# Performance work log

Hardware: AMD Instinct MI355X
Metric: run time of the kernel (lower is better)

## Reference

```python
import jax, jax.numpy as jnp
import numpy as np

B, L, D = 4, 4096, 1024
H = 16
BS = 64                      # block_size
HD = D // H                  # head_dim = 64
NB = L // BS                 # num_blocks = 64 (L multiple of BS -> no padding)
SCALE = HD ** -0.5
TEMP = 0.7
N_SINK_ITERS = 7


def setup_inputs() -> dict:
    key = jax.random.key(0)
    ks = jax.random.split(key, 7)
    x = jax.random.normal(ks[0], (B, L, D), dtype=jnp.float32)
    # gumbel noise matching torch.rand_like(log_alpha) -> -log(-log(u+eps)+eps)
    u = jax.random.uniform(ks[1], (B, H, NB, NB), dtype=jnp.float32)
    gumbel = -jnp.log(-jnp.log(u + 1e-20) + 1e-20)
    s_in = 1.0 / np.sqrt(D)
    W_qkv = jax.random.normal(ks[2], (D, 3 * D), dtype=jnp.float32) * s_in
    b_qkv = jnp.zeros((3 * D,), dtype=jnp.float32)
    W_out = jax.random.normal(ks[3], (D, D), dtype=jnp.float32) * s_in
    b_out = jnp.zeros((D,), dtype=jnp.float32)
    return {"x": x, "gumbel": gumbel, "W_qkv": W_qkv, "b_qkv": b_qkv,
            "W_out": W_out, "b_out": b_out}


def _sinkhorn(log_alpha):
    # Gumbel noise already added by caller; iterate row/col log-normalization.
    for _ in range(N_SINK_ITERS):
        log_alpha = log_alpha - jax.nn.logsumexp(log_alpha, axis=-1, keepdims=True)
        log_alpha = log_alpha - jax.nn.logsumexp(log_alpha, axis=-2, keepdims=True)
    return jnp.exp(log_alpha)


def reference(x, gumbel, W_qkv, b_qkv, W_out, b_out):
    qkv = x @ W_qkv + b_qkv                              # [B,L,3D]
    q, k, v = jnp.split(qkv, 3, axis=-1)

    def to_blocks(t):  # [B,L,D] -> [B,H,NB,BS,HD]
        return t.reshape(B, L, H, HD).transpose(0, 2, 1, 3).reshape(B, H, NB, BS, HD)

    q_b, k_b, v_b = to_blocks(q), to_blocks(k), to_blocks(v)

    # block summaries and Gumbel-Sinkhorn permutation over blocks
    q_repr = q_b.mean(axis=3)                            # [B,H,NB,HD]
    k_repr = k_b.mean(axis=3)
    sim = jnp.einsum('bhnd,bhmd->bhnm', q_repr, k_repr) * SCALE
    P = _sinkhorn((sim + gumbel) / TEMP)                 # [B,H,NB,NB]

    # sort K/V blocks via soft permutation
    k_flat = k_b.reshape(B, H, NB, BS * HD)
    v_flat = v_b.reshape(B, H, NB, BS * HD)
    k_sorted = jnp.einsum('bhnm,bhmf->bhnf', P, k_flat).reshape(B, H, NB, BS, HD)
    v_sorted = jnp.einsum('bhnm,bhmf->bhnf', P, v_flat).reshape(B, H, NB, BS, HD)

    # block i attends to [own block, sorted block i+1]; last block only to itself
    k_next = jnp.roll(k_sorted, -1, axis=2)
    v_next = jnp.roll(v_sorted, -1, axis=2)
    k_local = jnp.concatenate([k_b, k_next], axis=3)     # [B,H,NB,2BS,HD]
    v_local = jnp.concatenate([v_b, v_next], axis=3)

    scores = jnp.einsum('bhnqd,bhnkd->bhnqk', q_b, k_local) * SCALE
    # mask second half of keys for last block (it only attends to itself)
    scores = scores.at[:, :, -1, :, BS:].set(-1e9)
    attn = jax.nn.softmax(scores, axis=-1)               # dropout: eval -> identity
    out = jnp.einsum('bhnqk,bhnkd->bhnqd', attn, v_local)

    out = out.reshape(B, H, L, HD).transpose(0, 2, 1, 3).reshape(B, L, D)
    return out @ W_out + b_out
```

## Files before the change

### kernel.cpp

```cpp
#include <hip/hip_runtime.h>
#include <cstdint>
#include <cstddef>
#include <cstdio>

#define B_   4
#define L_   4096
#define D_   1024
#define H_   16
#define BS_  64
#define HD_  64
#define NB_  64
#define SCALE_   0.125f
#define INV_TEMP (1.0f/0.7f)

typedef unsigned short bf16_t;

#ifndef __has_builtin
#define __has_builtin(x) 0
#endif
#if __has_builtin(__builtin_amdgcn_global_load_lds)
#define HAS_GLD 1
#else
#define HAS_GLD 0
#endif

#if HAS_GLD
#define GLD16(gp, lp) __builtin_amdgcn_global_load_lds(                        \
    (__attribute__((address_space(1))) void*)(uintptr_t)(gp),                  \
    (__attribute__((address_space(3))) void*)(unsigned int)(uintptr_t)(lp),    \
    16, 0, 0)
#endif

__device__ __forceinline__ float b2f(bf16_t u) {
    union { unsigned int i; float f; } c; c.i = ((unsigned int)u) << 16; return c.f;
}
__device__ __forceinline__ bf16_t f2b(float f) {
    union { float f; unsigned int i; } c; c.f = f;
    unsigned int r = c.i + 0x7FFFu + ((c.i >> 16) & 1u);
    return (bf16_t)(r >> 16);
}

__device__ __forceinline__ void storeC(float* p, float v)  { *p = v; }
__device__ __forceinline__ void storeC(bf16_t* p, float v) { *p = f2b(v); }

using bf16x8 = __attribute__((ext_vector_type(8))) short;
using f32x4  = __attribute__((ext_vector_type(4))) float;

__global__ __launch_bounds__(256) void f32_to_bf16_kernel(
    const float* __restrict__ src, bf16_t* __restrict__ dst, int n4)
{
    const int i = blockIdx.x * 256 + threadIdx.x;
    if (i < n4) {
        float4 v = *(const float4*)(src + (size_t)i * 4);
        ushort4 o = {f2b(v.x), f2b(v.y), f2b(v.z), f2b(v.w)};
        *(ushort4*)(dst + (size_t)i * 4) = o;
    }
}

__global__ __launch_bounds__(256) void transpose_f32_bf16_kernel(
    const float* __restrict__ src, bf16_t* __restrict__ dst, int R, int C)
{
    __shared__ float t[32][33];
    const int c0 = blockIdx.x * 32, r0 = blockIdx.y * 32;
    for (int i = threadIdx.y; i < 32; i += 8)
        t[i][threadIdx.x] = src[(size_t)(r0 + i) * C + c0 + threadIdx.x];
    __syncthreads();
    for (int i = threadIdx.y; i < 32; i += 8)
        dst[(size_t)(c0 + i) * R + r0 + threadIdx.x] = f2b(t[threadIdx.x][i]);
}

#if HAS_GLD
#define SGA(tt, hb, dst)                                                       \
    GLD16(gAb + (size_t)((hb) * 128) * K + (size_t)(tt) * 64,                  \
          (dst) + (((hb) * 128 + w * 16) * 64));                               \
    GLD16(gAb + (size_t)((hb) * 128 + 8) * K + (size_t)(tt) * 64,              \
          (dst) + (((hb) * 128 + w * 16 + 8) * 64))
#define SGB(tt, hb, dst)                                                       \
    GLD16(gBb + (size_t)((hb) * 128) * K + (size_t)(tt) * 64,                  \
          (dst) + (((hb) * 128 + w * 16) * 64));                               \
    GLD16(gBb + (size_t)((hb) * 128 + 8) * K + (size_t)(tt) * 64,              \
          (dst) + (((hb) * 128 + w * 16 + 8) * 64))
#else
#define SGA(tt, hb, dst)                                                       \
    *(bf16x8*)((dst) + (((hb) * 128 + w * 16) * 64) + lane * 8) =              \
        *(const bf16x8*)(gAb + (size_t)((hb) * 128) * K + (size_t)(tt) * 64);  \
    *(bf16x8*)((dst) + (((hb) * 128 + w * 16 + 8) * 64) + lane * 8) =          \
        *(const bf16x8*)(gAb + (size_t)((hb) * 128 + 8) * K + (size_t)(tt) * 64)
#define SGB(tt, hb, dst)                                                       \
    *(bf16x8*)((dst) + (((hb) * 128 + w * 16) * 64) + lane * 8) =              \
        *(const bf16x8*)(gBb + (size_t)((hb) * 128) * K + (size_t)(tt) * 64);  \
    *(bf16x8*)((dst) + (((hb) * 128 + w * 16 + 8) * 64) + lane * 8) =          \
        *(const bf16x8*)(gBb + (size_t)((hb) * 128 + 8) * K + (size_t)(tt) * 64)
#endif

#define PHASE(ABUF, p, STAGE, ENDWAIT)                                         \
  {                                                                            \
    bf16x8 a0k0 = *(const bf16x8*)&(ABUF)[aRow0 + (2*(p))   * 1024 + csw[0]];  \
    bf16x8 a0k1 = *(const bf16x8*)&(ABUF)[aRow0 + (2*(p))   * 1024 + csw[1]];  \
    bf16x8 a1k0 = *(const bf16x8*)&(ABUF)[aRow0 + (2*(p)+1) * 1024 + csw[0]];  \
    bf16x8 a1k1 = *(const bf16x8*)&(ABUF)[aRow0 + (2*(p)+1) * 1024 + csw[1]];  \
    STAGE;                                                                     \
    __builtin_amdgcn_s_barrier();                                              \
    asm volatile("s_waitcnt lgkmcnt(0)" ::: "memory");                         \
    __builtin_amdgcn_s_setprio(1);                                             \
    _Pragma("unroll")                                                          \
    for (int fn = 0; fn < 4; ++fn) {                                           \
      acc[2*(p)][fn]   = __builtin_amdgcn_mfma_f32_16x16x32_bf16(              \
          a0k0, bq[fn][0], acc[2*(p)][fn], 0, 0, 0);                           \
      acc[2*(p)][fn]   = __builtin_amdgcn_mfma_f32_16x16x32_bf16(              \
          a0k1, bq[fn][1], acc[2*(p)][fn], 0, 0, 0);                           \
      acc[2*(p)+1][fn] = __builtin_amdgcn_mfma_f32_16x16x32_bf16(              \
          a1k0, bq[fn][0], acc[2*(p)+1][fn], 0, 0, 0);                         \
      acc[2*(p)+1][fn] = __builtin_amdgcn_mfma_f32_16x16x32_bf16(              \
          a1k1, bq[fn][1], acc[2*(p)+1][fn], 0, 0, 0);                         \
    }                                                                          \
    __builtin_amdgcn_s_setprio(0);                                             \
    ENDWAIT;                                                                   \
    __builtin_amdgcn_s_barrier();                                              \
    asm volatile("" ::: "memory");                                             \
  }

#define KTILE(ABUF, BBUF, NABUF, t)                                            \
  {                                                                            \
    bf16x8 bq[4][2];                                                           \
    _Pragma("unroll")                                                          \
    for (int fn = 0; fn < 4; ++fn) {                                           \
      bq[fn][0] = *(const bf16x8*)&(BBUF)[bRow0 + fn * 1024 + csw[0]];         \
      bq[fn][1] = *(const bf16x8*)&(BBUF)[bRow0 + fn * 1024 + csw[1]];         \
    }                                                                          \
    const bool stA = ((t) + 1 < KT), stB = ((t) + 2 < KT);                     \
    PHASE(ABUF, 0, if (stA) { SGA((t) + 1, 0, NABUF); }, )                     \
    PHASE(ABUF, 1, if (stA) { SGA((t) + 1, 1, NABUF); }, )                     \
    PHASE(ABUF, 2, if (stB) { SGB((t) + 2, 0, BBUF); }, )                      \
    PHASE(ABUF, 3, if (stB) { SGB((t) + 2, 1, BBUF); },                        \
          if ((t) + 1 < KT) {                                                  \
            if (stB) { asm volatile("s_waitcnt vmcnt(4)" ::: "memory"); }      \
            else     { asm volatile("s_waitcnt vmcnt(0)" ::: "memory"); }      \
          })                                                                   \
  }

template<typename TC>
__global__ __launch_bounds__(512, 2) void gemm256_8phase_kernel(
    const bf16_t* __restrict__ A, const bf16_t* __restrict__ Bt,
    const float* __restrict__ bias, TC* __restrict__ C,
    int M, int N, int K)
{
    __shared__ __align__(16) short sm[65536];
    short* const smA0 = sm;
    short* const smB0 = sm + 16384;
    short* const smA1 = sm + 32768;
    short* const smB1 = sm + 49152;

    const int tid  = threadIdx.x;
    const int lane = tid & 63;
    const int w    = tid >> 6;
    const int wr   = w >> 2, wc = w & 3;
    const int ml   = lane & 15, q2 = lane >> 4;

    const int gx  = gridDim.x;
    const int nwg = gx * gridDim.y;
    const int bid = blockIdx.y * gx + blockIdx.x;
    int swz = bid;
    if ((nwg & 7) == 0) swz = (bid & 7) * (nwg >> 3) + (bid >> 3);
    const int m0 = (swz / gx) * 256, n0 = (swz % gx) * 256;

    const int KT   = K >> 6;

    int csw[2];
    csw[0] = ((q2)     ^ (ml & 7)) * 8;
    csw[1] = ((4 + q2) ^ (ml & 7)) * 8;
    const int aRow0 = (wr * 128 + ml) * 64;
    const int bRow0 = (wc * 64  + ml) * 64;

    const int rl   = lane >> 3;
    const int scol = ((lane & 7) ^ rl) * 8;
    const bf16_t* gAb = A  + (size_t)(m0 + w * 16 + rl) * K + scol;
    const bf16_t* gBb = Bt + (size_t)(n0 + w * 16 + rl) * K + scol;

    f32x4 acc[8][4];
    #pragma unroll
    for (int i = 0; i < 8; ++i)
        #pragma unroll
        for (int j = 0; j < 4; ++j)
            acc[i][j] = {0.f, 0.f, 0.f, 0.f};

    SGA(0, 0, smA0); SGA(0, 1, smA0);
    SGB(0, 0, smB0); SGB(0, 1, smB0);
    SGB(1, 0, smB1); SGB(1, 1, smB1);
    asm volatile("s_waitcnt vmcnt(4)" ::: "memory");
    __builtin_amdgcn_s_barrier();
    asm volatile("" ::: "memory");

    for (int t = 0; t < KT; t += 2) {
        KTILE(smA0, smB0, smA1, t);
        KTILE(smA1, smB1, smA0, t + 1);
    }

    float bv[4];
    #pragma unroll
    for (int fn = 0; fn < 4; ++fn)
        bv[fn] = bias[n0 + wc * 64 + fn * 16 + ml];
    #pragma unroll
    for (int fm = 0; fm < 8; ++fm)
        #pragma unroll
        for (int fn = 0; fn < 4; ++fn)
            #pragma unroll
            for (int r = 0; r < 4; ++r) {
                const int row = m0 + wr * 128 + fm * 16 + q2 * 4 + r;
                const int col = n0 + wc * 64  + fn * 16 + ml;
                storeC(&C[(size_t)row * N + col], acc[fm][fn][r] + bv[fn]);
            }
}

#undef KTILE
#undef PHASE
#undef SGA
#undef SGB

__global__ __launch_bounds__(256) void block_repr_kernel(
    const bf16_t* __restrict__ qkv,
    float* __restrict__ q_repr, float* __restrict__ k_repr)
{
    __shared__ float red[2][4][64];
    const int blk = blockIdx.x;
    const int n  = blk & 63;
    const int bh = blk >> 6;
    const int h  = bh & 15, b = bh >> 4;
    const int d  = threadIdx.x & 63;
    const int ss = threadIdx.x >> 6;
    const bf16_t* base = qkv + (size_t)(b * L_ + n * BS_) * (3 * D_) + h * HD_ + d;
    float sq = 0.f, sk = 0.f;
    for (int s = ss; s < BS_; s += 4) {
        sq += b2f(base[(size_t)s * (3 * D_)]);
        sk += b2f(base[(size_t)s * (3 * D_) + D_]);
    }
    red[0][ss][d] = sq;
    red[1][ss][d] = sk;
    __syncthreads();
    if (threadIdx.x < 64) {
        const int dd = threadIdx.x;
        q_repr[(size_t)blk * HD_ + dd] =
            (red[0][0][dd] + red[0][1][dd] + red[0][2][dd] + red[0][3][dd])
            * (1.0f / BS_);
    } else if (threadIdx.x < 128) {
        const int dd = threadIdx.x - 64;
        k_repr[(size_t)blk * HD_ + dd] =
            (red[1][0][dd] + red[1][1][dd] + red[1][2][dd] + red[1][3][dd])
            * (1.0f / BS_);
    }
}

__global__ __launch_bounds__(256) void sinkhorn_kernel(
    const float* __restrict__ q_repr, const float* __restrict__ k_repr,
    const float* __restrict__ gumbel, bf16_t* __restrict__ P_bf)
{
    __shared__ __align__(16) float qr[64 * 68];
    __shared__ __align__(16) float kr[64 * 68];
    __shared__ float la[64 * 65];
    const int bh  = blockIdx.x;
    const int tid = threadIdx.x;
    const int r   = tid >> 2;
    const int sub = tid & 3;

    for (int idx = tid; idx < 4096; idx += 256) {
        const int rr = idx >> 6, cc = idx & 63;
        qr[rr * 68 + cc] = q_repr[(size_t)bh * 4096 + idx];
        kr[rr * 68 + cc] = k_repr[(size_t)bh * 4096 + idx];
    }
    __syncthreads();

    {
        float acc[16];
        #pragma unroll
        for (int mi = 0; mi < 16; ++mi) acc[mi] = 0.f;
        for (int d4 = 0; d4 < 16; ++d4) {
            const float4 q = *(const float4*)&qr[r * 68 + d4 * 4];
            #pragma unroll
            for (int mi = 0; mi < 16; ++mi) {
                const float4 kv = *(const float4*)&kr[(4 * mi + sub) * 68 + d4 * 4];
                acc[mi] += q.x * kv.x + q.y * kv.y + q.z * kv.z + q.w * kv.w;
            }
        }
        #pragma unroll
        for (int mi = 0; mi < 16; ++mi) {
            const int m = 4 * mi + sub;
            la[r * 65 + m] = (acc[mi] * SCALE_
                + gumbel[(size_t)bh * 4096 + r * 64 + m]) * INV_TEMP;
        }
    }
    __syncthreads();

    for (int it = 0; it < 7; ++it) {
        {
            float v[16];
            #pragma unroll
            for (int mi = 0; mi < 16; ++mi) v[mi] = la[r * 65 + 4 * mi + sub];
            float mx = v[0];
            #pragma unroll
            for (int mi = 1; mi < 16; ++mi) mx = fmaxf(mx, v[mi]);
            mx = fmaxf(mx, __shfl_xor(mx, 1, 64));
            mx = fmaxf(mx, __shfl_xor(mx, 2, 64));
            float sum = 0.f;
            #pragma unroll
            for (int mi = 0; mi < 16; ++mi) sum += expf(v[mi] - mx);
            sum += __shfl_xor(sum, 1, 64);
            sum += __shfl_xor(sum, 2, 64);
            const float lse = mx + logf(sum);
            #pragma unroll
            for (int mi = 0; mi < 16; ++mi) la[r * 65 + 4 * mi + sub] = v[mi] - lse;
        }
        __syncthreads();
        {
            float v[16];
            #pragma unroll
            for (int mi = 0; mi < 16; ++mi) v[mi] = la[(4 * mi + sub) * 65 + r];
            float mx = v[0];
            #pragma unroll
            for (int mi = 1; mi < 16; ++mi) mx = fmaxf(mx, v[mi]);
            mx = fmaxf(mx, __shfl_xor(mx, 1, 64));
            mx = fmaxf(mx, __shfl_xor(mx, 2, 64));
            float sum = 0.f;
            #pragma unroll
            for (int mi = 0; mi < 16; ++mi) sum += expf(v[mi] - mx);
            sum += __shfl_xor(sum, 1, 64);
            sum += __shfl_xor(sum, 2, 64);
            const float lse = mx + logf(sum);
            #pragma unroll
            for (int mi = 0; mi < 16; ++mi)
                la[(4 * mi + sub) * 65 + r] = v[mi] - lse;
        }
        __syncthreads();
    }

    #pragma unroll
    for (int mi = 0; mi < 16; ++mi) {
        const int m = 4 * mi + sub;
        P_bf[(size_t)bh * 4096 + r * 64 + m] = f2b(expf(la[r * 65 + m]));
    }
}

__global__ __launch_bounds__(256) void sort_kv_mfma_kernel(
    const bf16_t* __restrict__ P_bf, const bf16_t* __restrict__ qkv,
    bf16_t* __restrict__ k_sorted, bf16_t* __restrict__ v_sorted)
{
    constexpr int RS = 66;
    __shared__ __align__(16) short Kst[4 * 64 * RS];
    const int tid = threadIdx.x, lane = tid & 63, w = tid >> 6;
    const int bh = blockIdx.y;
    const int h = bh & 15, b = bh >> 4;
    const int c = blockIdx.x;
    const int ml = lane & 15, q8 = (lane >> 4) * 8;

    const bf16_t* ps = P_bf + (size_t)bh * (NB_ * NB_);

    const int s = c * 4 + w;
    const int fbase = c * 256 + w * 64;
    short* Kw = &Kst[w * 64 * RS];
    const int srow = lane >> 3;
    const int sc8  = (lane & 7) * 8;

    for (int kv = 0; kv < 2; ++kv) {
        const bf16_t* src = qkv + ((size_t)(b * L_ + s)) * (3 * D_)
                          + (kv ? 2 * D_ : 1 * D_) + h * HD_;

        #pragma unroll
        for (int g = 0; g < 8; ++g) {
            const int m = g * 8 + srow;
            *(bf16x8*)&Kw[m * RS + sc8] =
                *(const bf16x8*)(src + (size_t)m * (BS_ * 3 * D_) + sc8);
        }

        bf16x8 bt[4][2];
        #pragma unroll
        for (int kt = 0; kt < 2; ++kt)
            #pragma unroll
            for (int j = 0; j < 8; ++j) {
                const short* rp = &Kw[(kt * 32 + q8 + j) * RS + ml];
                #pragma unroll
                for (int t = 0; t < 4; ++t)
                    bt[t][kt][j] = rp[t * 16];
            }

        f32x4 acc[4][4];
        #pragma unroll
        for (int nt = 0; nt < 4; ++nt)
            #pragma unroll
            for (int t = 0; t < 4; ++t)
                acc[nt][t] = {0.f, 0.f, 0.f, 0.f};

        #pragma unroll
        for (int nt = 0; nt < 4; ++nt) {
            bf16x8 a0 = *(const bf16x8*)&ps[(size_t)(nt * 16 + ml) * 64 + q8];
            bf16x8 a1 = *(const bf16x8*)&ps[(size_t)(nt * 16 + ml) * 64 + 32 + q8];
            #pragma unroll
            for (int t = 0; t < 4; ++t) {
                acc[nt][t] = __builtin_amdgcn_mfma_f32_16x16x32_bf16(
                    a0, bt[t][0], acc[nt][t], 0, 0, 0);
                acc[nt][t] = __builtin_amdgcn_mfma_f32_16x16x32_bf16(
                    a1, bt[t][1], acc[nt][t], 0, 0, 0);
            }
        }

        bf16_t* dst = (kv ? v_sorted : k_sorted) + (size_t)bh * (NB_ * BS_ * HD_);
        const int quad4 = (lane >> 4) * 4;
        #pragma unroll
        for (int nt = 0; nt < 4; ++nt)
            #pragma unroll
            for (int t = 0; t < 4; ++t)
                #pragma unroll
                for (int r = 0; r < 4; ++r)
                    dst[(size_t)(nt * 16 + quad4 + r) * (BS_ * HD_)
                        + fbase + t * 16 + ml] = f2b(acc[nt][t][r]);
    }
}

__global__ __launch_bounds__(256) void attn_mfma_kernel(
    const bf16_t* __restrict__ qkv, const bf16_t* __restrict__ k_sorted,
    const bf16_t* __restrict__ v_sorted, bf16_t* __restrict__ attn_out)
{
    constexpr int KS = 72, VS = 136, PS = 136;
    __shared__ short Ks[128 * KS];
    __shared__ short Vt[64 * VS];
    short* const Psh = Ks;
    const int tid = threadIdx.x, lane = tid & 63, w = tid >> 6;
    const int n  = blockIdx.x & 63;
    const int bh = blockIdx.x >> 6;
    const int h = bh & 15, b = bh >> 4;
    const bool last = (n == NB_ - 1);

    const bf16_t* qb = qkv + (size_t)(b * L_ + n * BS_) * (3 * D_) + h * HD_;
    const bf16_t* kb = qb + D_;
    const bf16_t* vb = qb + 2 * D_;
    const size_t nextoff = ((size_t)bh * NB_ + (n + 1)) * (size_t)(BS_ * HD_);
    const bf16_t* kn = k_sorted + nextoff;
    const bf16_t* vn = v_sorted + nextoff;

    {
        const int col8 = (tid & 7) * 8, r0 = tid >> 3;
        const int jjmax = last ? 2 : 4;
        for (int jj = 0; jj < jjmax; ++jj) {
            const int row = jj * 32 + r0;
            const bf16_t* src = (row < 64)
                ? kb + (size_t)row * (3 * D_) + col8
                : kn + (size_t)(row - 64) * HD_ + col8;
            *(bf16x8*)&Ks[row * KS + col8] = *(const bf16x8*)src;
        }
    }
    {
        const int halves = last ? 1 : 2;
        for (int half = 0; half < halves; ++half) {
            for (int jj = 0; jj < 4; ++jj) {
                const int d0 = jj * 16 + w * 4;
                const bf16_t* src = (half == 0)
                    ? vb + (size_t)lane * (3 * D_) + d0
                    : vn + (size_t)lane * HD_ + d0;
                ushort4 u = *(const ushort4*)src;
                const int kcol = half * 64 + lane;
                Vt[(d0 + 0) * VS + kcol] = u.x;
                Vt[(d0 + 1) * VS + kcol] = u.y;
                Vt[(d0 + 2) * VS + kcol] = u.z;
                Vt[(d0 + 3) * VS + kcol] = u.w;
            }
        }
    }

    const int ml = lane & 15, quad = lane >> 4, q8 = quad * 8;
    const int m0 = w * 16;

    bf16x8 af0 = *(const bf16x8*)(qb + (size_t)(m0 + ml) * (3 * D_) + q8);
    bf16x8 af1 = *(const bf16x8*)(qb + (size_t)(m0 + ml) * (3 * D_) + 32 + q8);

    __syncthreads();

    const int ntile = last ? 4 : 8;
    f32x4 st[8];
    #pragma unroll
    for (int t = 0; t < 8; ++t) st[t] = {0.f, 0.f, 0.f, 0.f};
    for (int t = 0; t < ntile; ++t) {
        bf16x8 b0 = *(const bf16x8*)&Ks[(t * 16 + ml) * KS + q8];
        bf16x8 b1 = *(const bf16x8*)&Ks[(t * 16 + ml) * KS + 32 + q8];
        st[t] = __builtin_amdgcn_mfma_f32_16x16x32_bf16(af0, b0, st[t], 0, 0, 0);
        st[t] = __builtin_amdgcn_mfma_f32_16x16x32_bf16(af1, b1, st[t], 0, 0, 0);
    }

    __syncthreads();

    #pragma unroll
    for (int reg = 0; reg < 4; ++reg) {
        float mx = -1e30f;
        for (int t = 0; t < ntile; ++t) mx = fmaxf(mx, st[t][reg] * SCALE_);
        #pragma unroll
        for (int xm = 1; xm <= 8; xm <<= 1)
            mx = fmaxf(mx, __shfl_xor(mx, xm, 64));
        float e[8];
        float sum = 0.f;
        for (int t = 0; t < ntile; ++t) {
            e[t] = __expf(st[t][reg] * SCALE_ - mx);
            sum += e[t];
        }
        #pragma unroll
        for (int xm = 1; xm <= 8; xm <<= 1)
            sum += __shfl_xor(sum, xm, 64);
        const float inv = 1.0f / sum;
        const int qrow = m0 + quad * 4 + reg;
        for (int t = 0; t < ntile; ++t)
            Psh[qrow * PS + t * 16 + ml] = f2b(e[t] * inv);
    }

    __syncthreads();

    const int ktv = last ? 2 : 4;
    f32x4 oacc[4];
    #pragma unroll
    for (int t = 0; t < 4; ++t) oacc[t] = {0.f, 0.f, 0.f, 0.f};
    for (int kt = 0; kt < ktv; ++kt) {
        bf16x8 pa = *(const bf16x8*)&Psh[(m0 + ml) * PS + kt * 32 + q8];
        #pragma unroll
        for (int t = 0; t < 4; ++t) {
            bf16x8 vf = *(const bf16x8*)&Vt[(t * 16 + ml) * VS + kt * 32 + q8];
            oacc[t] = __builtin_amdgcn_mfma_f32_16x16x32_bf16(pa, vf, oacc[t], 0, 0, 0);
        }
    }

    bf16_t* ob = attn_out + (size_t)(b * L_ + n * BS_) * D_ + h * HD_;
    #pragma unroll
    for (int t = 0; t < 4; ++t)
        #pragma unroll
        for (int reg = 0; reg < 4; ++reg) {
            const int qrow = m0 + quad * 4 + reg;
            ob[(size_t)qrow * D_ + t * 16 + ml] = f2b(oacc[t][reg]);
        }
}

extern "C" void kernel_launch(void* const* d_in, const int* in_sizes, int n_in,
                              void* d_out, int out_size, void* d_ws, size_t ws_size,
                              hipStream_t stream)
{
    const float* x      = (const float*)d_in[0];
    const float* gumbel = (const float*)d_in[1];
    const float* W_qkv  = (const float*)d_in[2];
    const float* b_qkv  = (const float*)d_in[3];
    const float* W_out  = (const float*)d_in[4];
    const float* b_out  = (const float*)d_in[5];
    float* out = (float*)d_out;

    const size_t need = 204472320ull;
    if (ws_size < need) {
        fprintf(stderr, "[kernel_launch] ws_size=%zu < need=%zu — aborting launch\n",
                ws_size, need);
        return;
    }

    bf16_t* qkv      = (bf16_t*)d_ws;
    bf16_t* attn_o   = qkv    + (size_t)B_ * L_ * 3 * D_;
    bf16_t* k_sorted = attn_o + (size_t)B_ * L_ * D_;
    bf16_t* v_sorted = k_sorted + (size_t)B_ * L_ * D_;
    float* q_repr    = (float*)(v_sorted + (size_t)B_ * L_ * D_);
    float* k_repr    = q_repr + (size_t)B_ * H_ * NB_ * HD_;
    bf16_t* P_bf     = (bf16_t*)(k_repr + (size_t)B_ * H_ * NB_ * HD_);

    bf16_t* x_bf   = (bf16_t*)d_out;
    bf16_t* Wqkv_t = x_bf + (size_t)B_ * L_ * D_;
    bf16_t* Wout_t = (bf16_t*)q_repr;

    f32_to_bf16_kernel<<<(B_ * L_ * D_ / 4 + 255) / 256, 256, 0, stream>>>(
        x, x_bf, B_ * L_ * D_ / 4);
    transpose_f32_bf16_kernel<<<dim3(3 * D_ / 32, D_ / 32), dim3(32, 8), 0, stream>>>(
        W_qkv, Wqkv_t, D_, 3 * D_);

    gemm256_8phase_kernel<bf16_t>
        <<<dim3(3 * D_ / 256, B_ * L_ / 256), 512, 0, stream>>>(
        x_bf, Wqkv_t, b_qkv, qkv, B_ * L_, 3 * D_, D_);

    block_repr_kernel<<<B_ * H_ * NB_, 256, 0, stream>>>(qkv, q_repr, k_repr);

    sinkhorn_kernel<<<B_ * H_, 256, 0, stream>>>(q_repr, k_repr, gumbel, P_bf);

    sort_kv_mfma_kernel<<<dim3(16, B_ * H_), 256, 0, stream>>>(
        P_bf, qkv, k_sorted, v_sorted);

    attn_mfma_kernel<<<B_ * H_ * NB_, 256, 0, stream>>>(
        qkv, k_sorted, v_sorted, attn_o);

    transpose_f32_bf16_kernel<<<dim3(D_ / 32, D_ / 32), dim3(32, 8), 0, stream>>>(
        W_out, Wout_t, D_, D_);

    gemm256_8phase_kernel<float>
        <<<dim3(D_ / 256, B_ * L_ / 256), 512, 0, stream>>>(
        attn_o, Wout_t, b_out, out, B_ * L_, D_, D_);
}
```

Measured before the change: 414.1 us.

## Make GEMM persistent with next-tile prefetch and vectorize epilogue stores via MFMA operand swap

The QKV GEMM now runs as a persistent grid of 256 workgroups that each loop over 3 output tiles. The first K-tiles of the next output tile are prefetched into shared memory while the current tile's epilogue is written. Across the GEMM, sort and attention kernels, the MFMA A/B operands are swapped so each lane holds 4 consecutive columns of the result. This lets the epilogues use 4-wide vector stores and vector bias loads in place of scalar strided stores. The persistent loop adds register pressure and overlaps the prefetch with the store phase, and it depends on the tile swizzle staying correct when the tile counts change.

```diff
diff --git a/kernel.cpp b/kernel.cpp
--- a/kernel.cpp
+++ b/kernel.cpp
@@ -40,8 +40,12 @@
     return (bf16_t)(r >> 16);
 }
 
-__device__ __forceinline__ void storeC(float* p, float v)  { *p = v; }
-__device__ __forceinline__ void storeC(bf16_t* p, float v) { *p = f2b(v); }
+__device__ __forceinline__ void storeC4(float* p, float a, float b, float c, float d) {
+    *(float4*)p = float4{a, b, c, d};
+}
+__device__ __forceinline__ void storeC4(bf16_t* p, float a, float b, float c, float d) {
+    *(ushort4*)p = ushort4{f2b(a), f2b(b), f2b(c), f2b(d)};
+}
 
 using bf16x8 = __attribute__((ext_vector_type(8))) short;
 using f32x4  = __attribute__((ext_vector_type(4))) float;
@@ -106,13 +110,13 @@
     _Pragma("unroll")                                                          \
     for (int fn = 0; fn < 4; ++fn) {                                           \
       acc[2*(p)][fn]   = __builtin_amdgcn_mfma_f32_16x16x32_bf16(              \
-          a0k0, bq[fn][0], acc[2*(p)][fn], 0, 0, 0);                           \
+          bq[fn][0], a0k0, acc[2*(p)][fn], 0, 0, 0);                           \
       acc[2*(p)][fn]   = __builtin_amdgcn_mfma_f32_16x16x32_bf16(              \
-          a0k1, bq[fn][1], acc[2*(p)][fn], 0, 0, 0);                           \
+          bq[fn][1], a0k1, acc[2*(p)][fn], 0, 0, 0);                           \
       acc[2*(p)+1][fn] = __builtin_amdgcn_mfma_f32_16x16x32_bf16(              \
-          a1k0, bq[fn][0], acc[2*(p)+1][fn], 0, 0, 0);                         \
+          bq[fn][0], a1k0, acc[2*(p)+1][fn], 0, 0, 0);                         \
       acc[2*(p)+1][fn] = __builtin_amdgcn_mfma_f32_16x16x32_bf16(              \
-          a1k1, bq[fn][1], acc[2*(p)+1][fn], 0, 0, 0);                         \
+          bq[fn][1], a1k1, acc[2*(p)+1][fn], 0, 0, 0);                         \
     }                                                                          \
     __builtin_amdgcn_s_setprio(0);                                             \
     ENDWAIT;                                                                   \
@@ -143,7 +147,7 @@
 __global__ __launch_bounds__(512, 2) void gemm256_8phase_kernel(
     const bf16_t* __restrict__ A, const bf16_t* __restrict__ Bt,
     const float* __restrict__ bias, TC* __restrict__ C,
-    int M, int N, int K)
+    int M, int N, int K, int rounds)
 {
     __shared__ __align__(16) short sm[65536];
     short* const smA0 = sm;
@@ -157,14 +161,16 @@
     const int wr   = w >> 2, wc = w & 3;
     const int ml   = lane & 15, q2 = lane >> 4;
 
-    const int gx  = gridDim.x;
-    const int nwg = gx * gridDim.y;
-    const int bid = blockIdx.y * gx + blockIdx.x;
-    int swz = bid;
-    if ((nwg & 7) == 0) swz = (bid & 7) * (nwg >> 3) + (bid >> 3);
-    const int m0 = (swz / gx) * 256, n0 = (swz % gx) * 256;
-
+    const int nb   = gridDim.x;
+    const int ntil = nb * rounds;
+    const int gxt  = N >> 8;
     const int KT   = K >> 6;
+
+    auto tile_mn = [&](int tg, int& tm, int& tn) {
+        int swz = tg;
+        if ((ntil & 7) == 0) swz = (tg & 7) * (ntil >> 3) + (tg >> 3);
+        tm = (swz / gxt) * 256; tn = (swz % gxt) * 256;
+    };
 
     int csw[2];
     csw[0] = ((q2)     ^ (ml & 7)) * 8;
@@ -174,15 +180,13 @@
 
     const int rl   = lane >> 3;
     const int scol = ((lane & 7) ^ rl) * 8;
+
+    int m0, n0;
+    tile_mn(blockIdx.x, m0, n0);
     const bf16_t* gAb = A  + (size_t)(m0 + w * 16 + rl) * K + scol;
     const bf16_t* gBb = Bt + (size_t)(n0 + w * 16 + rl) * K + scol;
 
     f32x4 acc[8][4];
-    #pragma unroll
-    for (int i = 0; i < 8; ++i)
-        #pragma unroll
-        for (int j = 0; j < 4; ++j)
-            acc[i][j] = {0.f, 0.f, 0.f, 0.f};
 
     SGA(0, 0, smA0); SGA(0, 1, smA0);
     SGB(0, 0, smB0); SGB(0, 1, smB0);
@@ -191,25 +195,51 @@
     __builtin_amdgcn_s_barrier();
     asm volatile("" ::: "memory");
 
-    for (int t = 0; t < KT; t += 2) {
-        KTILE(smA0, smB0, smA1, t);
-        KTILE(smA1, smB1, smA0, t + 1);
-    }
-
-    float bv[4];
-    #pragma unroll
-    for (int fn = 0; fn < 4; ++fn)
-        bv[fn] = bias[n0 + wc * 64 + fn * 16 + ml];
-    #pragma unroll
-    for (int fm = 0; fm < 8; ++fm)
-        #pragma unroll
-        for (int fn = 0; fn < 4; ++fn)
-            #pragma unroll
-            for (int r = 0; r < 4; ++r) {
-                const int row = m0 + wr * 128 + fm * 16 + q2 * 4 + r;
-                const int col = n0 + wc * 64  + fn * 16 + ml;
-                storeC(&C[(size_t)row * N + col], acc[fm][fn][r] + bv[fn]);
+    for (int r = 0; ; ++r) {
+        #pragma unroll
+        for (int i = 0; i < 8; ++i)
+            #pragma unroll
+            for (int j = 0; j < 4; ++j)
+                acc[i][j] = {0.f, 0.f, 0.f, 0.f};
+
+        for (int t = 0; t < KT; t += 2) {
+            KTILE(smA0, smB0, smA1, t);
+            KTILE(smA1, smB1, smA0, t + 1);
+        }
+
+        const int em0 = m0, en0 = n0;
+        const bool more = (r + 1 < rounds);
+        if (more) {
+            tile_mn((r + 1) * nb + blockIdx.x, m0, n0);
+            gAb = A  + (size_t)(m0 + w * 16 + rl) * K + scol;
+            gBb = Bt + (size_t)(n0 + w * 16 + rl) * K + scol;
+            SGA(0, 0, smA0); SGA(0, 1, smA0);
+            SGB(0, 0, smB0); SGB(0, 1, smB0);
+            SGB(1, 0, smB1); SGB(1, 1, smB1);
+        }
+
+        float bv[4][4];
+        #pragma unroll
+        for (int fn = 0; fn < 4; ++fn) {
+            float4 bb = *(const float4*)&bias[en0 + wc * 64 + fn * 16 + q2 * 4];
+            bv[fn][0] = bb.x; bv[fn][1] = bb.y; bv[fn][2] = bb.z; bv[fn][3] = bb.w;
+        }
+        #pragma unroll
+        for (int fm = 0; fm < 8; ++fm)
+            #pragma unroll
+            for (int fn = 0; fn < 4; ++fn) {
+                const int row = em0 + wr * 128 + fm * 16 + ml;
+                const int col = en0 + wc * 64  + fn * 16 + q2 * 4;
+                storeC4(&C[(size_t)row * N + col],
+                        acc[fm][fn][0] + bv[fn][0], acc[fm][fn][1] + bv[fn][1],
+                        acc[fm][fn][2] + bv[fn][2], acc[fm][fn][3] + bv[fn][3]);
             }
+
+        if (!more) break;
+        asm volatile("s_waitcnt vmcnt(4)" ::: "memory");
+        __builtin_amdgcn_s_barrier();
+        asm volatile("" ::: "memory");
+    }
 }
 
 #undef KTILE
@@ -350,6 +380,7 @@
     const int h = bh & 15, b = bh >> 4;
     const int c = blockIdx.x;
     const int ml = lane & 15, q8 = (lane >> 4) * 8;
+    const int q4 = (lane >> 4) * 4;
 
     const bf16_t* ps = P_bf + (size_t)bh * (NB_ * NB_);
 
@@ -395,22 +426,21 @@
             #pragma unroll
             for (int t = 0; t < 4; ++t) {
                 acc[nt][t] = __builtin_amdgcn_mfma_f32_16x16x32_bf16(
-                    a0, bt[t][0], acc[nt][t], 0, 0, 0);
+                    bt[t][0], a0, acc[nt][t], 0, 0, 0);
                 acc[nt][t] = __builtin_amdgcn_mfma_f32_16x16x32_bf16(
-                    a1, bt[t][1], acc[nt][t], 0, 0, 0);
+                    bt[t][1], a1, acc[nt][t], 0, 0, 0);
             }
         }
 
         bf16_t* dst = (kv ? v_sorted : k_sorted) + (size_t)bh * (NB_ * BS_ * HD_);
-        const int quad4 = (lane >> 4) * 4;
         #pragma unroll
         for (int nt = 0; nt < 4; ++nt)
             #pragma unroll
             for (int t = 0; t < 4; ++t)
-                #pragma unroll
-                for (int r = 0; r < 4; ++r)
-                    dst[(size_t)(nt * 16 + quad4 + r) * (BS_ * HD_)
-                        + fbase + t * 16 + ml] = f2b(acc[nt][t][r]);
+                storeC4(&dst[(size_t)(nt * 16 + ml) * (BS_ * HD_)
+                             + fbase + t * 16 + q4],
+                        acc[nt][t][0], acc[nt][t][1],
+                        acc[nt][t][2], acc[nt][t][3]);
     }
 }
 
@@ -518,18 +548,15 @@
         #pragma unroll
         for (int t = 0; t < 4; ++t) {
             bf16x8 vf = *(const bf16x8*)&Vt[(t * 16 + ml) * VS + kt * 32 + q8];
-            oacc[t] = __builtin_amdgcn_mfma_f32_16x16x32_bf16(pa, vf, oacc[t], 0, 0, 0);
+            oacc[t] = __builtin_amdgcn_mfma_f32_16x16x32_bf16(vf, pa, oacc[t], 0, 0, 0);
         }
     }
 
     bf16_t* ob = attn_out + (size_t)(b * L_ + n * BS_) * D_ + h * HD_;
     #pragma unroll
     for (int t = 0; t < 4; ++t)
-        #pragma unroll
-        for (int reg = 0; reg < 4; ++reg) {
-            const int qrow = m0 + quad * 4 + reg;
-            ob[(size_t)qrow * D_ + t * 16 + ml] = f2b(oacc[t][reg]);
-        }
+        storeC4(&ob[(size_t)(m0 + ml) * D_ + t * 16 + quad * 4],
+                oacc[t][0], oacc[t][1], oacc[t][2], oacc[t][3]);
 }
 
 extern "C" void kernel_launch(void* const* d_in, const int* in_sizes, int n_in,
@@ -568,9 +595,8 @@
     transpose_f32_bf16_kernel<<<dim3(3 * D_ / 32, D_ / 32), dim3(32, 8), 0, stream>>>(
         W_qkv, Wqkv_t, D_, 3 * D_);
 
-    gemm256_8phase_kernel<bf16_t>
-        <<<dim3(3 * D_ / 256, B_ * L_ / 256), 512, 0, stream>>>(
-        x_bf, Wqkv_t, b_qkv, qkv, B_ * L_, 3 * D_, D_);
+    gemm256_8phase_kernel<bf16_t><<<256, 512, 0, stream>>>(
+        x_bf, Wqkv_t, b_qkv, qkv, B_ * L_, 3 * D_, D_, 3);
 
     block_repr_kernel<<<B_ * H_ * NB_, 256, 0, stream>>>(qkv, q_repr, k_repr);
 
@@ -585,7 +611,6 @@
     transpose_f32_bf16_kernel<<<dim3(D_ / 32, D_ / 32), dim3(32, 8), 0, stream>>>(
         W_out, Wout_t, D_, D_);
 
-    gemm256_8phase_kernel<float>
-        <<<dim3(D_ / 256, B_ * L_ / 256), 512, 0, stream>>>(
-        attn_o, Wout_t, b_out, out, B_ * L_, D_, D_);
-}
+    gemm256_8phase_kernel<float><<<256, 512, 0, stream>>>(
+        attn_o, Wout_t, b_out, out, B_ * L_, D_, D_, 1);
+}
```

Result: slower. 428.2 us (+3.4%).
